# Optimization experiments

Measured on AMD Instinct MI355X. Metric: run time of the kernel, lower is better.

## Reference

```python
import jax, jax.numpy as jnp
import numpy as np

EPS = 1e-5  # torch LayerNorm default

def layer_norm(v, gamma, beta):
    mu = jnp.mean(v, axis=-1, keepdims=True)
    var = jnp.mean(jnp.square(v - mu), axis=-1, keepdims=True)
    return (v - mu) * jax.lax.rsqrt(var + EPS) * gamma + beta

def setup_inputs() -> dict:
    key = jax.random.key(0)
    B, IN, H = 16384, 1024, 1024
    ks = jax.random.split(key, 6)
    # xavier_uniform for linear weights [out, in]
    def xavier(k, fan_out, fan_in):
        a = float(np.sqrt(6.0 / (fan_in + fan_out)))
        return jax.random.uniform(k, (fan_out, fan_in), jnp.float32, -a, a)
    return {
        "x": jax.random.normal(ks[0], (B, IN), jnp.float32),
        "h": jax.random.normal(ks[1], (B, H), jnp.float32),
        "c": jax.random.normal(ks[2], (B, H), jnp.float32),
        "W_i2h": xavier(ks[3], 4 * H, IN),
        "W_h2h": xavier(ks[4], 4 * H, H),
        "ln_i_g": jnp.ones((4 * H,), jnp.float32),
        "ln_i_b": jnp.zeros((4 * H,), jnp.float32),
        "ln_h_g": jnp.ones((4 * H,), jnp.float32),
        "ln_h_b": jnp.zeros((4 * H,), jnp.float32),
        "ln_c_g": jnp.ones((H,), jnp.float32),
        "ln_c_b": jnpp if False else jnp.zeros((H,), jnp.float32),
        "bias": jnp.zeros((4 * H,), jnp.float32),
    }

def reference(x, h, c, W_i2h, W_h2h, ln_i_g, ln_i_b, ln_h_g, ln_h_b, ln_c_g, ln_c_b, bias):
    i2h = jnp.einsum('bi,oi->bo', x, W_i2h)   # [B, 4H]
    h2h = jnp.einsum('bh,oh->bo', h, W_h2h)   # [B, 4H]
    logits = layer_norm(i2h, ln_i_g, ln_i_b) + layer_norm(h2h, ln_h_g, ln_h_b) + bias
    f, i, o, g = jnp.split(logits, 4, axis=-1)
    c_new = jax.nn.sigmoid(f) * c + jax.nn.sigmoid(i) * jnp.tanh(g)
    h_new = jax.nn.sigmoid(o) * jnp.tanh(layer_norm(c_new, ln_c_g, ln_c_b))
    return (h_new, c_new)
```

## Files before the change

### kernel.cpp

```cpp
#include <hip/hip_runtime.h>
#include <stdint.h>

typedef _Float16 f16;
typedef _Float16 f16x2 __attribute__((ext_vector_type(2)));
typedef _Float16 f16x4 __attribute__((ext_vector_type(4)));
typedef _Float16 f16x8 __attribute__((ext_vector_type(8)));
typedef float f32x4 __attribute__((ext_vector_type(4)));

#define AS1 __attribute__((address_space(1)))
#define AS3 __attribute__((address_space(3)))

__device__ __forceinline__ void gload_lds16(const f16* g, f16* l) {
    __builtin_amdgcn_global_load_lds((AS1 uint32_t*)g, (AS3 uint32_t*)l, 16, 0, 0);
}

__device__ __forceinline__ float fsig(float x) {
    return __builtin_amdgcn_rcpf(1.f + __builtin_amdgcn_exp2f(-1.44269504f * x));
}
__device__ __forceinline__ float ftanh(float x) {
    return 2.f * __builtin_amdgcn_rcpf(1.f + __builtin_amdgcn_exp2f(-2.88539008f * x)) - 1.f;
}
__device__ __forceinline__ float wave_sum(float v) {
#pragma unroll
    for (int off = 32; off >= 1; off >>= 1) v += __shfl_xor(v, off, 64);
    return v;
}

__global__ __launch_bounds__(256) void convert_kernel(
    const float* __restrict__ x, const float* __restrict__ h,
    const float* __restrict__ wi, const float* __restrict__ wh,
    f16* __restrict__ dst) {
    const int64_t NX = 16777216, NW = 4194304;
    int64_t g8 = ((int64_t)blockIdx.x * 256 + threadIdx.x) * 8;
    const float* src;
    int64_t off;
    if (g8 < NX)               { src = x;  off = g8; }
    else if (g8 < 2 * NX)      { src = h;  off = g8 - NX; }
    else if (g8 < 2 * NX + NW) { src = wi; off = g8 - 2 * NX; }
    else                       { src = wh; off = g8 - 2 * NX - NW; }
    f32x4 v0 = *(const f32x4*)(src + off);
    f32x4 v1 = *(const f32x4*)(src + off + 4);
    f16x8 o = { (f16)v0.x, (f16)v0.y, (f16)v0.z, (f16)v0.w,
                (f16)v1.x, (f16)v1.y, (f16)v1.z, (f16)v1.w };
    *(f16x8*)(dst + g8) = o;
}

__global__ __launch_bounds__(256, 2) void gemm_bt_f16(
    const f16* __restrict__ Abase, const f16* __restrict__ Bbase,
    f16* __restrict__ Cbase) {
    const int K = 1024, N = 4096, M = 16384;
    const int z = blockIdx.z;
    const f16* A = Abase + (int64_t)z * M * K;
    const f16* B = Bbase + (int64_t)z * N * K;
    f16* C = Cbase + (int64_t)z * (int64_t)M * N;

    __shared__ f16 sA[128 * 64];
    __shared__ f16 sB[128 * 64];

    const int tid = threadIdx.x;
    const int wave = tid >> 6;
    const int lane = tid & 63;
    const int wm = (wave >> 1) * 64;
    const int wn = (wave & 1) * 64;
    const int bm = blockIdx.y * 128;
    const int bn = blockIdx.x * 128;

    const int srow = lane >> 3;
    const int sp   = lane & 7;

    const int quad = lane >> 4;
    const int l16  = lane & 15;

    f32x4 acc[4][4];
#pragma unroll
    for (int i = 0; i < 4; i++)
#pragma unroll
        for (int j = 0; j < 4; j++) acc[i][j] = (f32x4){0.f, 0.f, 0.f, 0.f};

    for (int k0 = 0; k0 < K; k0 += 64) {
#pragma unroll
        for (int i = 0; i < 4; i++) {
            int rowbase = wave * 32 + i * 8;
            int r = rowbase + srow;
            int c = sp ^ (r & 7);
            gload_lds16(A + (int64_t)(bm + r) * K + (k0 + c * 8), &sA[rowbase * 64]);
            gload_lds16(B + (int64_t)(bn + r) * K + (k0 + c * 8), &sB[rowbase * 64]);
        }
        __syncthreads();

#pragma unroll
        for (int ks = 0; ks < 2; ks++) {
            f16x8 a[4], b[4];
#pragma unroll
            for (int mt = 0; mt < 4; mt++) {
                int r = wm + mt * 16 + l16;
                int pp = (ks * 4 + quad) ^ (r & 7);
                a[mt] = *(const f16x8*)&sA[r * 64 + pp * 8];
            }
#pragma unroll
            for (int nt = 0; nt < 4; nt++) {
                int r = wn + nt * 16 + l16;
                int pp = (ks * 4 + quad) ^ (r & 7);
                b[nt] = *(const f16x8*)&sB[r * 64 + pp * 8];
            }
#pragma unroll
            for (int mt = 0; mt < 4; mt++)
#pragma unroll
                for (int nt = 0; nt < 4; nt++)
                    acc[mt][nt] = __builtin_amdgcn_mfma_f32_16x16x32_f16(
                        a[mt], b[nt], acc[mt][nt], 0, 0, 0);
        }
        __syncthreads();
    }

#pragma unroll
    for (int mt = 0; mt < 4; mt++) {
#pragma unroll
        for (int nt = 0; nt < 4; nt++) {
#pragma unroll
            for (int r = 0; r < 4; r++) {
                int row = bm + wm + mt * 16 + quad * 4 + r;
                int col = bn + wn + nt * 16 + l16;
                C[(int64_t)row * N + col] = (f16)acc[mt][nt][r];
            }
        }
    }
}

__global__ __launch_bounds__(256) void lstm_fuse(
    const f16* __restrict__ i2h, const f16* __restrict__ h2h,
    const float* __restrict__ c,
    const float* __restrict__ gi, const float* __restrict__ bi,
    const float* __restrict__ gh, const float* __restrict__ bh,
    const float* __restrict__ gc, const float* __restrict__ bc,
    const float* __restrict__ bias,
    float* __restrict__ hout, float* __restrict__ cout) {
    const int tid  = threadIdx.x;
    const int row  = blockIdx.x * 2 + (tid >> 7);
    const int t    = tid & 127;
    const int wave = tid >> 6;
    const int lane = tid & 63;
    const int j0   = t * 8;

    const f16* pi = i2h + (int64_t)row * 4096;
    const f16* ph = h2h + (int64_t)row * 4096;

    f16x8 av[4], bv[4];
#pragma unroll
    for (int q = 0; q < 4; q++) {
        av[q] = *(const f16x8*)(pi + q * 1024 + j0);
        bv[q] = *(const f16x8*)(ph + q * 1024 + j0);
    }

    const f16x2 ones = { (f16)1.f, (f16)1.f };
    float si = 0.f, ssi = 0.f, sh = 0.f, ssh = 0.f;
#pragma unroll
    for (int q = 0; q < 4; q++) {
#pragma unroll
        for (int p = 0; p < 4; p++) {
            f16x2 a2 = { av[q][2 * p], av[q][2 * p + 1] };
            f16x2 b2 = { bv[q][2 * p], bv[q][2 * p + 1] };
            si  = __builtin_amdgcn_fdot2(a2, ones, si, false);
            ssi = __builtin_amdgcn_fdot2(a2, a2, ssi, false);
            sh  = __builtin_amdgcn_fdot2(b2, ones, sh, false);
            ssh = __builtin_amdgcn_fdot2(b2, b2, ssh, false);
        }
    }

    __shared__ float red[4][4];
    si = wave_sum(si); ssi = wave_sum(ssi); sh = wave_sum(sh); ssh = wave_sum(ssh);
    if (lane == 0) { red[wave][0] = si; red[wave][1] = ssi; red[wave][2] = sh; red[wave][3] = ssh; }
    __syncthreads();
    const int wb = wave & 2;
    si  = red[wb][0] + red[wb + 1][0];
    ssi = red[wb][1] + red[wb + 1][1];
    sh  = red[wb][2] + red[wb + 1][2];
    ssh = red[wb][3] + red[wb + 1][3];

    const float inv4096 = 1.0f / 4096.0f;
    float mi  = si * inv4096;
    float rsi = __builtin_amdgcn_rsqf(ssi * inv4096 - mi * mi + 1e-5f);
    float mh  = sh * inv4096;
    float rsh = __builtin_amdgcn_rsqf(ssh * inv4096 - mh * mh + 1e-5f);

    float lgf[8], lgi_[8], lgo[8], lgg[8];
    float* lgq[4] = { lgf, lgi_, lgo, lgg };
#pragma unroll
    for (int q = 0; q < 4; q++) {
#pragma unroll
        for (int g4 = 0; g4 < 2; g4++) {
            int jj = q * 1024 + j0 + g4 * 4;
            f32x4 giv = *(const f32x4*)(gi + jj);
            f32x4 biv = *(const f32x4*)(bi + jj);
            f32x4 ghv = *(const f32x4*)(gh + jj);
            f32x4 bhv = *(const f32x4*)(bh + jj);
            f32x4 bbv = *(const f32x4*)(bias + jj);
#pragma unroll
            for (int u = 0; u < 4; u++) {
                float t1 = rsi * giv[u];
                float t2 = rsh * ghv[u];
                float base = biv[u] + bhv[u] + bbv[u] - mi * t1 - mh * t2;
                lgq[q][g4 * 4 + u] =
                    (float)av[q][g4 * 4 + u] * t1 + (float)bv[q][g4 * 4 + u] * t2 + base;
            }
        }
    }

    f32x4 cv0 = *(const f32x4*)(c + (int64_t)row * 1024 + j0);
    f32x4 cv1 = *(const f32x4*)(c + (int64_t)row * 1024 + j0 + 4);
    float cn[8];
    float sc = 0.f, ssc = 0.f;
#pragma unroll
    for (int u = 0; u < 8; u++) {
        float cvu = (u < 4) ? cv0[u & 3] : cv1[u & 3];
        float fg = fsig(lgf[u]);
        float ig = fsig(lgi_[u]);
        float gg = ftanh(lgg[u]);
        float v = fg * cvu + ig * gg;
        cn[u] = v; sc += v; ssc += v * v;
    }

    __shared__ float red2[4][2];
    sc = wave_sum(sc); ssc = wave_sum(ssc);
    if (lane == 0) { red2[wave][0] = sc; red2[wave][1] = ssc; }
    __syncthreads();
    sc  = red2[wb][0] + red2[wb + 1][0];
    ssc = red2[wb][1] + red2[wb + 1][1];

    const float inv1024 = 1.0f / 1024.0f;
    float mc  = sc * inv1024;
    float rsc = __builtin_amdgcn_rsqf(ssc * inv1024 - mc * mc + 1e-5f);

    f32x4 gc0 = *(const f32x4*)(gc + j0);
    f32x4 gc1 = *(const f32x4*)(gc + j0 + 4);
    f32x4 bc0 = *(const f32x4*)(bc + j0);
    f32x4 bc1 = *(const f32x4*)(bc + j0 + 4);
    f32x4 h0, h1, c0, c1;
#pragma unroll
    for (int u = 0; u < 8; u++) {
        float gcv = (u < 4) ? gc0[u & 3] : gc1[u & 3];
        float bcv = (u < 4) ? bc0[u & 3] : bc1[u & 3];
        float og  = fsig(lgo[u]);
        float lnc = (cn[u] - mc) * rsc * gcv + bcv;
        float hv  = og * ftanh(lnc);
        if (u < 4) { h0[u & 3] = hv; c0[u & 3] = cn[u]; }
        else       { h1[u & 3] = hv; c1[u & 3] = cn[u]; }
    }
    float* hp = hout + (int64_t)row * 1024 + j0;
    float* cp = cout + (int64_t)row * 1024 + j0;
    *(f32x4*)hp       = h0;
    *(f32x4*)(hp + 4) = h1;
    *(f32x4*)cp       = c0;
    *(f32x4*)(cp + 4) = c1;
}

extern "C" void kernel_launch(void* const* d_in, const int* in_sizes, int n_in,
                              void* d_out, int out_size, void* d_ws, size_t ws_size,
                              hipStream_t stream) {
    const float* x      = (const float*)d_in[0];
    const float* h      = (const float*)d_in[1];
    const float* c      = (const float*)d_in[2];
    const float* wi     = (const float*)d_in[3];
    const float* wh     = (const float*)d_in[4];
    const float* ln_i_g = (const float*)d_in[5];
    const float* ln_i_b = (const float*)d_in[6];
    const float* ln_h_g = (const float*)d_in[7];
    const float* ln_h_b = (const float*)d_in[8];
    const float* ln_c_g = (const float*)d_in[9];
    const float* ln_c_b = (const float*)d_in[10];
    const float* bias   = (const float*)d_in[11];

    f16* ws16     = (f16*)d_ws;
    f16* xh16     = ws16;
    f16* w16      = ws16 + 33554432;
    f16* logits16 = ws16 + 41943040;

    convert_kernel<<<20480, 256, 0, stream>>>(x, h, wi, wh, ws16);
    gemm_bt_f16<<<dim3(32, 128, 2), 256, 0, stream>>>(xh16, w16, logits16);

    float* hout = (float*)d_out;
    float* cout = hout + 16777216;
    lstm_fuse<<<8192, 256, 0, stream>>>(logits16, logits16 + 67108864, c,
                                        ln_i_g, ln_i_b, ln_h_g, ln_h_b,
                                        ln_c_g, ln_c_b, bias, hout, cout);
}
```

Measured before the change: 691.1 us.

## Rewrite GEMM as 256x256 tile, 8-wave, multi-phase pipelined kernel

Replaces the 128x128 single-buffered GEMM with a 256x256 tile computed by 8 waves. K slices are double-buffered into LDS with async global-to-LDS loads and four phases per iteration, each interleaving fragment loads, staging of the next slice, and prioritized MFMA bursts under explicit barriers. It also adds a workgroup swizzle for L2 locality, swaps the MFMA operand order so each lane stores f16x4 vectors, and uses an XOR swizzle on the LDS layout. The aim is to hide memory latency behind MFMA and raise arithmetic intensity, in exchange for more registers and fragile hand-written vmcnt accounting.

```diff
diff --git a/kernel.cpp b/kernel.cpp
--- a/kernel.cpp
+++ b/kernel.cpp
@@ -45,84 +45,141 @@
     *(f16x8*)(dst + g8) = o;
 }
 
-__global__ __launch_bounds__(256, 2) void gemm_bt_f16(
+__global__ __launch_bounds__(512, 2) void gemm_8ph_f16(
     const f16* __restrict__ Abase, const f16* __restrict__ Bbase,
     f16* __restrict__ Cbase) {
-    const int K = 1024, N = 4096, M = 16384;
+    const int K = 1024, N = 4096;
+    const int64_t M = 16384;
     const int z = blockIdx.z;
     const f16* A = Abase + (int64_t)z * M * K;
-    const f16* B = Bbase + (int64_t)z * N * K;
-    f16* C = Cbase + (int64_t)z * (int64_t)M * N;
-
-    __shared__ f16 sA[128 * 64];
-    __shared__ f16 sB[128 * 64];
-
-    const int tid = threadIdx.x;
+    const f16* B = Bbase + (int64_t)z * (int64_t)N * K;
+    f16* C = Cbase + (int64_t)z * M * N;
+
+    __shared__ f16 sA[2][2][256][32];
+    __shared__ f16 sB[2][2][256][32];
+
+    const int tid  = threadIdx.x;
     const int wave = tid >> 6;
     const int lane = tid & 63;
-    const int wm = (wave >> 1) * 64;
-    const int wn = (wave & 1) * 64;
-    const int bm = blockIdx.y * 128;
-    const int bn = blockIdx.x * 128;
-
-    const int srow = lane >> 3;
-    const int sp   = lane & 7;
-
-    const int quad = lane >> 4;
+    const int q    = lane >> 4;
     const int l16  = lane & 15;
-
-    f32x4 acc[4][4];
-#pragma unroll
-    for (int i = 0; i < 4; i++)
-#pragma unroll
-        for (int j = 0; j < 4; j++) acc[i][j] = (f32x4){0.f, 0.f, 0.f, 0.f};
-
-    for (int k0 = 0; k0 < K; k0 += 64) {
-#pragma unroll
-        for (int i = 0; i < 4; i++) {
-            int rowbase = wave * 32 + i * 8;
-            int r = rowbase + srow;
-            int c = sp ^ (r & 7);
-            gload_lds16(A + (int64_t)(bm + r) * K + (k0 + c * 8), &sA[rowbase * 64]);
-            gload_lds16(B + (int64_t)(bn + r) * K + (k0 + c * 8), &sB[rowbase * 64]);
+    const int wm   = (wave >> 2) * 128;
+    const int wn   = (wave & 3) * 64;
+
+    const int wg  = blockIdx.y * 16 + blockIdx.x;
+    const int swz = (wg & 7) * 128 + (wg >> 3);
+    const int bm = (swz >> 4) * 256;
+    const int bn = (swz & 15) * 256;
+
+    const f16* Ab = A + (int64_t)bm * K;
+    const f16* Bb = B + (int64_t)bn * K;
+
+    const int srow = lane >> 2;
+    const int sg   = ((lane & 3) ^ ((lane >> 3) & 3)) * 8;
+    const int p8   = (q ^ ((l16 >> 1) & 3)) * 8;
+
+    f32x4 acc[8][4];
+#pragma unroll
+    for (int i = 0; i < 8; ++i)
+#pragma unroll
+        for (int j = 0; j < 4; ++j) acc[i][j] = (f32x4){0.f, 0.f, 0.f, 0.f};
+
+    f16x8 afr[4], bfr[4];
+
+    auto STAGE = [&](const f16* __restrict__ gb, f16* plane, int kpos) {
+#pragma unroll
+        for (int i = 0; i < 2; ++i) {
+            const int rowbase = i * 128 + wave * 16;
+            gload_lds16(gb + (rowbase + srow) * 1024 + kpos + sg,
+                        plane + rowbase * 32);
         }
-        __syncthreads();
-
-#pragma unroll
-        for (int ks = 0; ks < 2; ks++) {
-            f16x8 a[4], b[4];
-#pragma unroll
-            for (int mt = 0; mt < 4; mt++) {
-                int r = wm + mt * 16 + l16;
-                int pp = (ks * 4 + quad) ^ (r & 7);
-                a[mt] = *(const f16x8*)&sA[r * 64 + pp * 8];
-            }
-#pragma unroll
-            for (int nt = 0; nt < 4; nt++) {
-                int r = wn + nt * 16 + l16;
-                int pp = (ks * 4 + quad) ^ (r & 7);
-                b[nt] = *(const f16x8*)&sB[r * 64 + pp * 8];
-            }
-#pragma unroll
-            for (int mt = 0; mt < 4; mt++)
-#pragma unroll
-                for (int nt = 0; nt < 4; nt++)
-                    acc[mt][nt] = __builtin_amdgcn_mfma_f32_16x16x32_f16(
-                        a[mt], b[nt], acc[mt][nt], 0, 0, 0);
-        }
-        __syncthreads();
-    }
-
-#pragma unroll
-    for (int mt = 0; mt < 4; mt++) {
-#pragma unroll
-        for (int nt = 0; nt < 4; nt++) {
-#pragma unroll
-            for (int r = 0; r < 4; r++) {
-                int row = bm + wm + mt * 16 + quad * 4 + r;
-                int col = bn + wn + nt * 16 + l16;
-                C[(int64_t)row * N + col] = (f16)acc[mt][nt][r];
-            }
+    };
+    auto LDA = [&](const f16* plane, int msub) {
+#pragma unroll
+        for (int i = 0; i < 4; ++i)
+            afr[i] = *(const f16x8*)(plane + (wm + msub * 64 + i * 16 + l16) * 32 + p8);
+    };
+    auto LDB = [&](const f16* plane) {
+#pragma unroll
+        for (int i = 0; i < 4; ++i)
+            bfr[i] = *(const f16x8*)(plane + (wn + i * 16 + l16) * 32 + p8);
+    };
+    auto MFMA = [&](int msub) {
+        __builtin_amdgcn_s_setprio(1);
+#pragma unroll
+        for (int mi = 0; mi < 4; ++mi)
+#pragma unroll
+            for (int ni = 0; ni < 4; ++ni)
+                acc[msub * 4 + mi][ni] = __builtin_amdgcn_mfma_f32_16x16x32_f16(
+                    bfr[ni], afr[mi], acc[msub * 4 + mi][ni], 0, 0, 0);
+        __builtin_amdgcn_s_setprio(0);
+    };
+
+    STAGE(Ab, &sA[0][0][0][0], 0);
+    STAGE(Bb, &sB[0][0][0][0], 0);
+    STAGE(Ab, &sA[0][1][0][0], 32);
+    STAGE(Bb, &sB[0][1][0][0], 32);
+    STAGE(Ab, &sA[1][0][0][0], 64);
+    STAGE(Bb, &sB[1][0][0][0], 64);
+    asm volatile("s_waitcnt vmcnt(8)" ::: "memory");
+    __builtin_amdgcn_s_barrier();
+
+#pragma unroll 1
+    for (int t = 0; t < 16; ++t) {
+        const int buf = t & 1;
+        const f16* A0 = &sA[buf][0][0][0];
+        const f16* A1 = &sA[buf][1][0][0];
+        const f16* B0 = &sB[buf][0][0][0];
+        const f16* B1 = &sB[buf][1][0][0];
+
+        LDB(B0);
+        LDA(A0, 0);
+        if (t < 15) STAGE(Ab, &sA[buf ^ 1][1][0][0], (t + 1) * 64 + 32);
+        __builtin_amdgcn_s_barrier();
+        asm volatile("s_waitcnt lgkmcnt(0)" ::: "memory");
+        __builtin_amdgcn_sched_barrier(0);
+        MFMA(0);
+        __builtin_amdgcn_s_barrier();
+
+        LDA(A0, 1);
+        if (t < 15) STAGE(Bb, &sB[buf ^ 1][1][0][0], (t + 1) * 64 + 32);
+        __builtin_amdgcn_s_barrier();
+        asm volatile("s_waitcnt lgkmcnt(0)" ::: "memory");
+        __builtin_amdgcn_sched_barrier(0);
+        MFMA(1);
+        if (t < 15) asm volatile("s_waitcnt vmcnt(8)" ::: "memory");
+        else        asm volatile("s_waitcnt vmcnt(0)" ::: "memory");
+        __builtin_amdgcn_s_barrier();
+
+        LDB(B1);
+        LDA(A1, 0);
+        if (t < 14) STAGE(Ab, &sA[buf][0][0][0], (t + 2) * 64);
+        __builtin_amdgcn_s_barrier();
+        asm volatile("s_waitcnt lgkmcnt(0)" ::: "memory");
+        __builtin_amdgcn_sched_barrier(0);
+        MFMA(0);
+        __builtin_amdgcn_s_barrier();
+
+        LDA(A1, 1);
+        if (t < 14) STAGE(Bb, &sB[buf][0][0][0], (t + 2) * 64);
+        __builtin_amdgcn_s_barrier();
+        asm volatile("s_waitcnt lgkmcnt(0)" ::: "memory");
+        __builtin_amdgcn_sched_barrier(0);
+        MFMA(1);
+        if (t < 14)       asm volatile("s_waitcnt vmcnt(8)" ::: "memory");
+        else if (t == 14) asm volatile("s_waitcnt vmcnt(4)" ::: "memory");
+        __builtin_amdgcn_s_barrier();
+    }
+
+#pragma unroll
+    for (int mt = 0; mt < 8; ++mt) {
+        const int row = bm + wm + mt * 16 + l16;
+        f16* crow = C + (int64_t)row * N + bn + wn + q * 4;
+#pragma unroll
+        for (int nt = 0; nt < 4; ++nt) {
+            f16x4 v = { (f16)acc[mt][nt][0], (f16)acc[mt][nt][1],
+                        (f16)acc[mt][nt][2], (f16)acc[mt][nt][3] };
+            *(f16x4*)(crow + nt * 16) = v;
         }
     }
 }
@@ -276,7 +333,7 @@
     f16* logits16 = ws16 + 41943040;
 
     convert_kernel<<<20480, 256, 0, stream>>>(x, h, wi, wh, ws16);
-    gemm_bt_f16<<<dim3(32, 128, 2), 256, 0, stream>>>(xh16, w16, logits16);
+    gemm_8ph_f16<<<dim3(16, 64, 2), 512, 0, stream>>>(xh16, w16, logits16);
 
     float* hout = (float*)d_out;
     float* cout = hout + 16777216;
```

After: 743.5 us. 7.6% more time.
